# Optimization experiments

Hardware: AMD Instinct MI355X
Metric: run time of the kernel (lower is better)

## Reference

```python
import jax, jax.numpy as jnp
import numpy as np

B, HF, WF = 64, 14, 14
E, D, H, EM, V, L = 2048, 256, 256, 256, 10000, 32


def setup_inputs() -> dict:
    key = jax.random.key(0)
    ks = jax.random.split(key, 16)
    s = lambda k, shape: jax.random.normal(k, shape, jnp.float32) * 0.02
    lengths = jnp.clip(jax.random.randint(ks[2], (B, 1), 2, L + 1), 2, L)
    lengths = lengths.at[0, 0].set(L)  # ensure max target length == L-1 (static)
    return {
        "image_feature": jax.random.normal(ks[0], (B, HF, WF, E), jnp.float32),
        "caption_token": jax.random.randint(ks[1], (B, L), 0, V),
        "caption_length": lengths,
        "Wf": s(ks[3], (E, H)), "bf": jnp.zeros((H,), jnp.float32),
        "Wh": s(ks[4], (D, H)), "bh": jnp.zeros((H,), jnp.float32),
        "We": s(ks[5], (H, 1)), "be": jnp.zeros((1,), jnp.float32),
        "emb": jax.random.uniform(ks[6], (V, EM), jnp.float32, -0.1, 0.1),
        "W_ih": s(ks[7], (EM + E, 4 * D)), "b_ih": jnp.zeros((4 * D,), jnp.float32),
        "W_hh": s(ks[8], (D, 4 * D)), "b_hh": jnp.zeros((4 * D,), jnp.float32),
        "W_hid": s(ks[9], (E, D)), "b_hid": jnp.zeros((D,), jnp.float32),
        "W_cell": s(ks[10], (E, D)), "b_cell": jnp.zeros((D,), jnp.float32),
        "W_gate": s(ks[11], (D, E)), "b_gate": jnp.zeros((E,), jnp.float32),
        "W_head": jax.random.uniform(ks[12], (D, V), jnp.float32, -0.1, 0.1),
        "b_head": jnp.zeros((V,), jnp.float32),
    }


def reference(image_feature, caption_token, caption_length,
              Wf, bf, Wh, bh, We, be, emb,
              W_ih, b_ih, W_hh, b_hh,
              W_hid, b_hid, W_cell, b_cell,
              W_gate, b_gate, W_head, b_head):
    feat = image_feature.reshape(image_feature.shape[0], -1, image_feature.shape[-1])  # [B,P,E]
    lengths = caption_length[:, 0]
    order = jnp.argsort(-lengths)               # descending, stable
    feat = feat[order]
    tok = caption_token[order]
    target = lengths[order] - 1                 # [B] target lengths
    T = tok.shape[1] - 1                        # static max target length

    mean_feat = feat.mean(axis=1)               # [B,E]
    h0 = mean_feat @ W_hid + b_hid              # init hidden
    c0 = mean_feat @ W_cell + b_cell            # init cell
    cap_emb = emb[tok]                          # [B,L,EM] teacher-forcing embeds
    fe = feat @ Wf + bf                         # [B,P,H] feature proj (loop-invariant)

    def step(carry, t):
        h, c = carry
        m = (target > t)[:, None].astype(h.dtype)        # active-row mask (block_size)
        # additive attention
        he = (h @ Wh + bh)[:, None, :]                   # [B,1,H]
        e = jax.nn.relu(fe + he) @ We + be               # [B,P,1]
        w = jax.nn.softmax(e, axis=1)                    # over pixels
        ctx = (w * feat).sum(axis=1)                     # [B,E]
        # sigmoid gate on context
        ctx = jax.nn.sigmoid(h @ W_gate + b_gate) * ctx
        # LSTMCell (torch gate order i,f,g,o)
        x = jnp.concatenate([cap_emb[:, t], ctx], axis=1)
        g = x @ W_ih + b_ih + h @ W_hh + b_hh
        i, f, gg, o = jnp.split(g, 4, axis=1)
        c_new = jax.nn.sigmoid(f) * c + jax.nn.sigmoid(i) * jnp.tanh(gg)
        h_new = jax.nn.sigmoid(o) * jnp.tanh(c_new)
        pred = h_new @ W_head + b_head                   # dropout = identity (eval)
        h = jnp.where(m > 0, h_new, h)
        c = jnp.where(m > 0, c_new, c)
        return (h, c), (pred * m, w[:, :, 0] * m)

    _, (preds, weights) = jax.lax.scan(step, (h0, c0), jnp.arange(T))
    caption_prediction = jnp.transpose(preds, (1, 0, 2))   # [B,T,V]
    attention_weight = jnp.transpose(weights, (1, 0, 2))   # [B,T,P]
    return caption_prediction, attention_weight
```

## Files before the change

kernel.cpp:

```cpp
#include <hip/hip_runtime.h>
#include <math.h>

#define B 64
#define P 196
#define E 2048
#define D 256
#define H_ 256
#define EM 256
#define V 10000
#define L 32
#define T 31
#define KX 2560

__global__ __launch_bounds__(64) void sort_kernel(const int* __restrict__ clen,
                                                  int* __restrict__ order,
                                                  int* __restrict__ target) {
    __shared__ int len_s[B];
    int i = threadIdx.x;
    len_s[i] = clen[i];
    __syncthreads();
    int li = len_s[i];
    int rank = 0;
    for (int j = 0; j < B; ++j) {
        int lj = len_s[j];
        if (lj > li || (lj == li && j < i)) rank++;
    }
    order[rank] = i;
    target[rank] = li - 1;
}

__global__ __launch_bounds__(256) void mean_kernel(const float* __restrict__ feat,
                                                   const int* __restrict__ order,
                                                   float* __restrict__ mean_feat) {
    int b = blockIdx.x;
    int e = blockIdx.y * 256 + threadIdx.x;
    int src = order[b];
    const float* fp = feat + (size_t)src * P * E + e;
    float acc = 0.f;
    #pragma unroll 4
    for (int p = 0; p < P; ++p) acc += fp[(size_t)p * E];
    mean_feat[b * E + e] = acc * (1.0f / (float)P);
}

__global__ __launch_bounds__(256) void h0c0_gemm(const float* __restrict__ mean_feat,
                                                 const float* __restrict__ W_hid,
                                                 const float* __restrict__ W_cell,
                                                 float* __restrict__ hpart) {
    __shared__ float As[32][68];
    __shared__ float Bs[32][64];
    int cb = blockIdx.x;
    int ky = blockIdx.y;
    int tid = threadIdx.x;
    int tx = tid & 15, ty = tid >> 4;
    const float* Wsrc;
    int ncol0;
    if (cb < 4) { Wsrc = W_hid;  ncol0 = cb * 64; }
    else        { Wsrc = W_cell; ncol0 = (cb - 4) * 64; }
    float acc[4][4] = {};
    for (int k0 = ky * 256; k0 < ky * 256 + 256; k0 += 32) {
        #pragma unroll
        for (int q = 0; q < 2; ++q) {
            int idx = q * 256 + tid;
            int kv = idx & 7, m = idx >> 3;
            float4 v = *(const float4*)(mean_feat + (size_t)m * E + k0 + kv * 4);
            As[kv * 4 + 0][m] = v.x;
            As[kv * 4 + 1][m] = v.y;
            As[kv * 4 + 2][m] = v.z;
            As[kv * 4 + 3][m] = v.w;
        }
        #pragma unroll
        for (int q = 0; q < 2; ++q) {
            int idx = q * 256 + tid;
            int n4 = idx & 15, kk = idx >> 4;
            float4 v = *(const float4*)(Wsrc + (size_t)(k0 + kk) * 256 + ncol0 + n4 * 4);
            *(float4*)&Bs[kk][n4 * 4] = v;
        }
        __syncthreads();
        #pragma unroll
        for (int kk = 0; kk < 32; ++kk) {
            float4 av = *(const float4*)&As[kk][ty * 4];
            float4 bv = *(const float4*)&Bs[kk][tx * 4];
            acc[0][0] += av.x * bv.x; acc[0][1] += av.x * bv.y; acc[0][2] += av.x * bv.z; acc[0][3] += av.x * bv.w;
            acc[1][0] += av.y * bv.x; acc[1][1] += av.y * bv.y; acc[1][2] += av.y * bv.z; acc[1][3] += av.y * bv.w;
            acc[2][0] += av.z * bv.x; acc[2][1] += av.z * bv.y; acc[2][2] += av.z * bv.z; acc[2][3] += av.z * bv.w;
            acc[3][0] += av.w * bv.x; acc[3][1] += av.w * bv.y; acc[3][2] += av.w * bv.z; acc[3][3] += av.w * bv.w;
        }
        __syncthreads();
    }
    #pragma unroll
    for (int a = 0; a < 4; ++a) {
        int row = ty * 4 + a;
        float4 o = {acc[a][0], acc[a][1], acc[a][2], acc[a][3]};
        *(float4*)(hpart + ((size_t)ky * B + row) * 512 + cb * 64 + tx * 4) = o;
    }
}

__global__ __launch_bounds__(256) void h0c0_reduce(const float* __restrict__ hpart,
                                                   const float* __restrict__ b_hid,
                                                   const float* __restrict__ b_cell,
                                                   const float* __restrict__ emb,
                                                   const int* __restrict__ cap_tok,
                                                   const int* __restrict__ order,
                                                   float* __restrict__ h,
                                                   float* __restrict__ c,
                                                   float* __restrict__ xbuf) {
    int b = blockIdx.x, tid = threadIdx.x;
    float s0 = 0.f, s1 = 0.f;
    #pragma unroll
    for (int ky = 0; ky < 8; ++ky) {
        const float* hp = hpart + ((size_t)ky * B + b) * 512;
        s0 += hp[tid];
        s1 += hp[256 + tid];
    }
    float h0 = s0 + b_hid[tid];
    h[b * D + tid] = h0;
    c[b * D + tid] = s1 + b_cell[tid];
    xbuf[(size_t)b * KX + 2304 + tid] = h0;
    int tok0 = cap_tok[order[b] * L + 0];
    xbuf[(size_t)b * KX + tid] = emb[(size_t)tok0 * EM + tid];
}

__global__ __launch_bounds__(256) void fe_gemm(const float* __restrict__ feat,
                                               const int* __restrict__ order,
                                               const float* __restrict__ Wf,
                                               const float* __restrict__ bf,
                                               float* __restrict__ fe) {
    __shared__ float As[32][68];
    __shared__ float Bs[32][64];
    __shared__ int srcRow[64];
    int rowBlock = blockIdx.x;
    int colBlock = blockIdx.y;
    int tid = threadIdx.x;
    if (tid < 64) {
        int gr = rowBlock * 64 + tid;
        int b = gr / P, p = gr % P;
        srcRow[tid] = order[b] * P + p;
    }
    __syncthreads();
    int tx = tid & 15, ty = tid >> 4;
    float acc[4][4] = {};
    for (int k0 = 0; k0 < E; k0 += 32) {
        #pragma unroll
        for (int q = 0; q < 2; ++q) {
            int idx = q * 256 + tid;
            int kv = idx & 7, m = idx >> 3;
            float4 v = *(const float4*)(feat + (size_t)srcRow[m] * E + k0 + kv * 4);
            As[kv * 4 + 0][m] = v.x;
            As[kv * 4 + 1][m] = v.y;
            As[kv * 4 + 2][m] = v.z;
            As[kv * 4 + 3][m] = v.w;
        }
        {
            int n4 = tid & 15, kk = tid >> 4;
            float4 v = *(const float4*)(Wf + (size_t)(k0 + kk) * H_ + colBlock * 64 + n4 * 4);
            *(float4*)&Bs[kk][n4 * 4] = v;
            int kk2 = kk + 16;
            float4 v2 = *(const float4*)(Wf + (size_t)(k0 + kk2) * H_ + colBlock * 64 + n4 * 4);
            *(float4*)&Bs[kk2][n4 * 4] = v2;
        }
        __syncthreads();
        #pragma unroll
        for (int kk = 0; kk < 32; ++kk) {
            float4 av = *(const float4*)&As[kk][ty * 4];
            float4 bv = *(const float4*)&Bs[kk][tx * 4];
            acc[0][0] += av.x * bv.x; acc[0][1] += av.x * bv.y; acc[0][2] += av.x * bv.z; acc[0][3] += av.x * bv.w;
            acc[1][0] += av.y * bv.x; acc[1][1] += av.y * bv.y; acc[1][2] += av.y * bv.z; acc[1][3] += av.y * bv.w;
            acc[2][0] += av.z * bv.x; acc[2][1] += av.z * bv.y; acc[2][2] += av.z * bv.z; acc[2][3] += av.z * bv.w;
            acc[3][0] += av.w * bv.x; acc[3][1] += av.w * bv.y; acc[3][2] += av.w * bv.z; acc[3][3] += av.w * bv.w;
        }
        __syncthreads();
    }
    float4 bias = *(const float4*)(bf + colBlock * 64 + tx * 4);
    #pragma unroll
    for (int a = 0; a < 4; ++a) {
        int gr = rowBlock * 64 + ty * 4 + a;
        float4 o;
        o.x = acc[a][0] + bias.x;
        o.y = acc[a][1] + bias.y;
        o.z = acc[a][2] + bias.z;
        o.w = acc[a][3] + bias.w;
        *(float4*)(fe + (size_t)gr * H_ + colBlock * 64 + tx * 4) = o;
    }
}

__global__ __launch_bounds__(256) void attn_pw(const int* __restrict__ target,
                                               const float* __restrict__ gpart,
                                               const float* __restrict__ b_ih,
                                               const float* __restrict__ b_hh,
                                               const float* __restrict__ emb,
                                               const int* __restrict__ cap_tok,
                                               const int* __restrict__ order,
                                               const float* __restrict__ Wh,
                                               const float* __restrict__ bh,
                                               const float* __restrict__ We,
                                               const float* __restrict__ be,
                                               const float* __restrict__ fe,
                                               float* __restrict__ h,
                                               float* __restrict__ c,
                                               float* __restrict__ hn_all,
                                               float* __restrict__ xbuf,
                                               float* __restrict__ wbuf,
                                               float* __restrict__ out2,
                                               int t) {
    int b = blockIdx.x;
    int tgt = target[b];
    bool pw_active = (t > 0) && (tgt > t - 1);
    bool at_active = (tgt > t);
    if (!pw_active && !at_active) return;
    __shared__ float hs[D];
    __shared__ float hes[D];
    __shared__ float es[P];
    __shared__ float red[4];
    int tid = threadIdx.x;
    if (pw_active) {
        int d = tid;
        float gi = b_ih[d] + b_hh[d];
        float gf = b_ih[D + d] + b_hh[D + d];
        float gg = b_ih[2 * D + d] + b_hh[2 * D + d];
        float go = b_ih[3 * D + d] + b_hh[3 * D + d];
        #pragma unroll
        for (int ky = 0; ky < 8; ++ky) {
            const float* gp = gpart + ((size_t)ky * B + b) * 1024;
            gi += gp[d];
            gf += gp[D + d];
            gg += gp[2 * D + d];
            go += gp[3 * D + d];
        }
        float c_old = c[b * D + d];
        float si = 1.f / (1.f + expf(-gi));
        float sf = 1.f / (1.f + expf(-gf));
        float so = 1.f / (1.f + expf(-go));
        float cn = sf * c_old + si * tanhf(gg);
        float hnv = so * tanhf(cn);
        c[b * D + d] = cn;
        h[b * D + d] = hnv;
        hs[d] = hnv;
        hn_all[((size_t)(t - 1) * B + b) * D + d] = hnv;
        xbuf[(size_t)b * KX + 2304 + d] = hnv;
        int tokn = cap_tok[order[b] * L + t];
        xbuf[(size_t)b * KX + d] = emb[(size_t)tokn * EM + d];
    } else {
        hs[tid] = h[b * D + tid];
    }
    __syncthreads();
    if (!at_active) return;
    float acc = 0.f;
    #pragma unroll 8
    for (int k = 0; k < D; ++k) acc += hs[k] * Wh[(size_t)k * H_ + tid];
    hes[tid] = acc + bh[tid];
    __syncthreads();
    int wave = tid >> 6, lane = tid & 63;
    float4 he4 = *(const float4*)&hes[lane * 4];
    float4 we4 = *(const float4*)(We + lane * 4);
    for (int p = wave; p < P; p += 4) {
        float4 fv = *(const float4*)(fe + ((size_t)b * P + p) * H_ + lane * 4);
        float x0 = fv.x + he4.x; x0 = x0 > 0.f ? x0 : 0.f;
        float x1 = fv.y + he4.y; x1 = x1 > 0.f ? x1 : 0.f;
        float x2 = fv.z + he4.z; x2 = x2 > 0.f ? x2 : 0.f;
        float x3 = fv.w + he4.w; x3 = x3 > 0.f ? x3 : 0.f;
        float s = x0 * we4.x + x1 * we4.y + x2 * we4.z + x3 * we4.w;
        #pragma unroll
        for (int off = 32; off > 0; off >>= 1) s += __shfl_down(s, off);
        if (lane == 0) es[p] = s + be[0];
    }
    __syncthreads();
    float mx = -1e30f;
    for (int p = tid; p < P; p += 256) mx = fmaxf(mx, es[p]);
    #pragma unroll
    for (int off = 32; off > 0; off >>= 1) mx = fmaxf(mx, __shfl_down(mx, off));
    if (lane == 0) red[wave] = mx;
    __syncthreads();
    mx = fmaxf(fmaxf(red[0], red[1]), fmaxf(red[2], red[3]));
    __syncthreads();
    float sum = 0.f;
    for (int p = tid; p < P; p += 256) {
        float ex = expf(es[p] - mx);
        es[p] = ex;
        sum += ex;
    }
    #pragma unroll
    for (int off = 32; off > 0; off >>= 1) sum += __shfl_down(sum, off);
    if (lane == 0) red[wave] = sum;
    __syncthreads();
    sum = red[0] + red[1] + red[2] + red[3];
    float inv = 1.0f / sum;
    for (int p = tid; p < P; p += 256) {
        float wv = es[p] * inv;
        wbuf[b * P + p] = wv;
        out2[((size_t)b * T + t) * P + p] = wv;
    }
}

__global__ __launch_bounds__(256) void ctx_kernel(const float* __restrict__ feat,
                                                  const int* __restrict__ order,
                                                  const float* __restrict__ wbuf,
                                                  const float* __restrict__ W_gate,
                                                  const float* __restrict__ b_gate,
                                                  const float* __restrict__ h,
                                                  const int* __restrict__ target,
                                                  float* __restrict__ xbuf,
                                                  int t) {
    int b = blockIdx.x;
    if (target[b] <= t) return;
    int y = blockIdx.y;
    __shared__ float ws_[P];
    __shared__ float hs[D];
    __shared__ float4 rc[3][64];
    __shared__ float4 rg[3][64];
    int tid = threadIdx.x;
    if (tid < P) ws_[tid] = wbuf[b * P + tid];
    hs[tid] = h[b * D + tid];
    __syncthreads();
    int c4 = tid & 63, q = tid >> 6;
    int src = order[b];
    const float4* f4 = (const float4*)(feat + (size_t)src * P * E) + y * 64 + c4;
    float4 acc = {0.f, 0.f, 0.f, 0.f};
    for (int p = q * 49; p < q * 49 + 49; ++p) {
        float w = ws_[p];
        float4 fv = f4[(size_t)p * 512];
        acc.x += w * fv.x; acc.y += w * fv.y; acc.z += w * fv.z; acc.w += w * fv.w;
    }
    const float4* g4 = (const float4*)W_gate + y * 64 + c4;
    float4 gacc = {0.f, 0.f, 0.f, 0.f};
    for (int k = q * 64; k < q * 64 + 64; ++k) {
        float hv = hs[k];
        float4 wv = g4[(size_t)k * 512];
        gacc.x += hv * wv.x; gacc.y += hv * wv.y; gacc.z += hv * wv.z; gacc.w += hv * wv.w;
    }
    if (q) { rc[q - 1][c4] = acc; rg[q - 1][c4] = gacc; }
    __syncthreads();
    if (q == 0) {
        #pragma unroll
        for (int j = 0; j < 3; ++j) {
            float4 a = rc[j][c4], g = rg[j][c4];
            acc.x += a.x; acc.y += a.y; acc.z += a.z; acc.w += a.w;
            gacc.x += g.x; gacc.y += g.y; gacc.z += g.z; gacc.w += g.w;
        }
        float4 gb = *(const float4*)(b_gate + (y * 64 + c4) * 4);
        float4 o;
        o.x = acc.x / (1.f + expf(-(gacc.x + gb.x)));
        o.y = acc.y / (1.f + expf(-(gacc.y + gb.y)));
        o.z = acc.z / (1.f + expf(-(gacc.z + gb.z)));
        o.w = acc.w / (1.f + expf(-(gacc.w + gb.w)));
        *(float4*)(xbuf + (size_t)b * KX + EM + (y * 64 + c4) * 4) = o;
    }
}

__global__ __launch_bounds__(256) void lstm_gemm(const float* __restrict__ xbuf,
                                                 const float* __restrict__ W_ih,
                                                 const float* __restrict__ W_hh,
                                                 float* __restrict__ gpart) {
    __shared__ float As[32][68];
    __shared__ float Bs[32][64];
    int cb = blockIdx.x;
    int ky = blockIdx.y;
    int tid = threadIdx.x;
    int tx = tid & 15, ty = tid >> 4;
    float acc[4][4] = {};
    int k0base = ky * 320;
    for (int k0 = k0base; k0 < k0base + 320; k0 += 32) {
        #pragma unroll
        for (int q = 0; q < 2; ++q) {
            int idx = q * 256 + tid;
            int kv = idx & 7, m = idx >> 3;
            float4 v = *(const float4*)(xbuf + (size_t)m * KX + k0 + kv * 4);
            As[kv * 4 + 0][m] = v.x;
            As[kv * 4 + 1][m] = v.y;
            As[kv * 4 + 2][m] = v.z;
            As[kv * 4 + 3][m] = v.w;
        }
        #pragma unroll
        for (int q = 0; q < 2; ++q) {
            int idx = q * 256 + tid;
            int n4 = idx & 15, kk = idx >> 4;
            int k = k0 + kk;
            const float* src = (k < EM + E) ? (W_ih + (size_t)k * 1024)
                                            : (W_hh + (size_t)(k - EM - E) * 1024);
            float4 v = *(const float4*)(src + cb * 64 + n4 * 4);
            *(float4*)&Bs[kk][n4 * 4] = v;
        }
        __syncthreads();
        #pragma unroll
        for (int kk = 0; kk < 32; ++kk) {
            float4 av = *(const float4*)&As[kk][ty * 4];
            float4 bv = *(const float4*)&Bs[kk][tx * 4];
            acc[0][0] += av.x * bv.x; acc[0][1] += av.x * bv.y; acc[0][2] += av.x * bv.z; acc[0][3] += av.x * bv.w;
            acc[1][0] += av.y * bv.x; acc[1][1] += av.y * bv.y; acc[1][2] += av.y * bv.z; acc[1][3] += av.y * bv.w;
            acc[2][0] += av.z * bv.x; acc[2][1] += av.z * bv.y; acc[2][2] += av.z * bv.z; acc[2][3] += av.z * bv.w;
            acc[3][0] += av.w * bv.x; acc[3][1] += av.w * bv.y; acc[3][2] += av.w * bv.z; acc[3][3] += av.w * bv.w;
        }
        __syncthreads();
    }
    #pragma unroll
    for (int a = 0; a < 4; ++a) {
        int bidx = ty * 4 + a;
        float4 o = {acc[a][0], acc[a][1], acc[a][2], acc[a][3]};
        *(float4*)(gpart + ((size_t)ky * B + bidx) * 1024 + cb * 64 + tx * 4) = o;
    }
}

__global__ __launch_bounds__(256) void head_batch(const float* __restrict__ hn_all,
                                                  const float* __restrict__ W_head,
                                                  const float* __restrict__ b_head,
                                                  const int* __restrict__ target,
                                                  float* __restrict__ out1) {
    int by = blockIdx.y;
    int t = by >> 1, qh = by & 1;
    if (target[qh * 32] <= t) return;
    __shared__ float hs[32][260];
    int cb = blockIdx.x;
    int tid = threadIdx.x;
    #pragma unroll
    for (int q = 0; q < 8; ++q) {
        int idx = q * 256 + tid;
        int r = idx >> 6, kq = idx & 63;
        float4 v = *(const float4*)(hn_all + ((size_t)t * B + qh * 32 + r) * D + kq * 4);
        *(float4*)&hs[r][kq * 4] = v;
    }
    __syncthreads();
    int col = cb * 64 + (tid & 63);
    int rgrp = (tid >> 6) * 8;
    if (col < V) {
        float acc[8] = {};
        for (int kq = 0; kq < 64; ++kq) {
            float w0 = W_head[(size_t)(kq * 4 + 0) * V + col];
            float w1 = W_head[(size_t)(kq * 4 + 1) * V + col];
            float w2 = W_head[(size_t)(kq * 4 + 2) * V + col];
            float w3 = W_head[(size_t)(kq * 4 + 3) * V + col];
            #pragma unroll
            for (int r = 0; r < 8; ++r) {
                float4 hv = *(const float4*)&hs[rgrp + r][kq * 4];
                acc[r] += hv.x * w0 + hv.y * w1 + hv.z * w2 + hv.w * w3;
            }
        }
        float bh_ = b_head[col];
        #pragma unroll
        for (int r = 0; r < 8; ++r) {
            int brow = qh * 32 + rgrp + r;
            if (target[brow] > t)
                out1[((size_t)brow * T + t) * V + col] = acc[r] + bh_;
        }
    }
}

extern "C" void kernel_launch(void* const* d_in, const int* in_sizes, int n_in,
                              void* d_out, int out_size, void* d_ws, size_t ws_size,
                              hipStream_t stream) {
    const float* feat   = (const float*)d_in[0];
    const int*   tok    = (const int*)d_in[1];
    const int*   clen   = (const int*)d_in[2];
    const float* Wf     = (const float*)d_in[3];
    const float* bf     = (const float*)d_in[4];
    const float* Wh     = (const float*)d_in[5];
    const float* bh     = (const float*)d_in[6];
    const float* We     = (const float*)d_in[7];
    const float* be     = (const float*)d_in[8];
    const float* emb    = (const float*)d_in[9];
    const float* W_ih   = (const float*)d_in[10];
    const float* b_ih   = (const float*)d_in[11];
    const float* W_hh   = (const float*)d_in[12];
    const float* b_hh   = (const float*)d_in[13];
    const float* W_hid  = (const float*)d_in[14];
    const float* b_hid  = (const float*)d_in[15];
    const float* W_cell = (const float*)d_in[16];
    const float* b_cell = (const float*)d_in[17];
    const float* W_gate = (const float*)d_in[18];
    const float* b_gate = (const float*)d_in[19];
    const float* W_head = (const float*)d_in[20];
    const float* b_head = (const float*)d_in[21];

    float* out1 = (float*)d_out;
    float* out2 = out1 + (size_t)B * T * V;

    char* wp = (char*)d_ws;
    int* order   = (int*)wp;           wp += 256;
    int* targetp = (int*)wp;           wp += 256;
    float* fe    = (float*)wp;         wp += (size_t)B * P * H_ * sizeof(float);
    float* hbuf  = (float*)wp;         wp += (size_t)B * D * sizeof(float);
    float* cbuf  = (float*)wp;         wp += (size_t)B * D * sizeof(float);
    float* wbuf  = (float*)wp;         wp += (size_t)B * P * sizeof(float);
    float* xbuf  = (float*)wp;         wp += (size_t)B * KX * sizeof(float);
    float* gpart = (float*)wp;         wp += (size_t)8 * B * 1024 * sizeof(float);
    float* mean_feat = (float*)wp;     wp += (size_t)B * E * sizeof(float);
    float* hpart = (float*)wp;         wp += (size_t)8 * B * 512 * sizeof(float);
    float* hn_all = (float*)wp;        wp += (size_t)T * B * D * sizeof(float);

    hipMemsetAsync(d_out, 0, (size_t)out_size * sizeof(float), stream);

    sort_kernel<<<1, 64, 0, stream>>>(clen, order, targetp);
    mean_kernel<<<dim3(B, E / 256), 256, 0, stream>>>(feat, order, mean_feat);
    h0c0_gemm<<<dim3(8, 8), 256, 0, stream>>>(mean_feat, W_hid, W_cell, hpart);
    h0c0_reduce<<<B, 256, 0, stream>>>(hpart, b_hid, b_cell, emb, tok, order,
                                       hbuf, cbuf, xbuf);
    fe_gemm<<<dim3(196, 4), 256, 0, stream>>>(feat, order, Wf, bf, fe);

    for (int t = 0; t < T; ++t) {
        attn_pw<<<B, 256, 0, stream>>>(targetp, gpart, b_ih, b_hh, emb, tok, order,
                                       Wh, bh, We, be, fe, hbuf, cbuf, hn_all,
                                       xbuf, wbuf, out2, t);
        ctx_kernel<<<dim3(B, 8), 256, 0, stream>>>(feat, order, wbuf, W_gate, b_gate,
                                                   hbuf, targetp, xbuf, t);
        lstm_gemm<<<dim3(16, 8), 256, 0, stream>>>(xbuf, W_ih, W_hh, gpart);
    }
    attn_pw<<<B, 256, 0, stream>>>(targetp, gpart, b_ih, b_hh, emb, tok, order,
                                   Wh, bh, We, be, fe, hbuf, cbuf, hn_all,
                                   xbuf, wbuf, out2, T);
    head_batch<<<dim3(157, 62), 256, 0, stream>>>(hn_all, W_head, b_head, targetp, out1);
}
```

Measured before the change: 2.873 ms.

## Fuse all stages into one persistent cooperative kernel with grid syncs

Replaces the many per-timestep kernel launches with a single cooperative persistent kernel that loops over phases, separated by grid-wide syncs. The fe GEMM and mean reduction run in the same phase, and the output head projection for step t-1 is overlapped with the LSTM GEMM of step t rather than done as one batched GEMM at the end. The fe tile is widened to 64x128. This removes launch overhead across the 31-step recurrence. In exchange it depends on grid.sync cost and on a grid size capped at 512 blocks, which limits parallelism in the large GEMM phases.

```diff
diff --git a/kernel.cpp b/kernel.cpp
--- a/kernel.cpp
+++ b/kernel.cpp
@@ -1,5 +1,8 @@
 #include <hip/hip_runtime.h>
+#include <hip/hip_cooperative_groups.h>
 #include <math.h>
+
+namespace cg = cooperative_groups;
 
 #define B 64
 #define P 196
@@ -12,78 +15,112 @@
 #define T 31
 #define KX 2560
 
-__global__ __launch_bounds__(64) void sort_kernel(const int* __restrict__ clen,
-                                                  int* __restrict__ order,
-                                                  int* __restrict__ target) {
-    __shared__ int len_s[B];
-    int i = threadIdx.x;
-    len_s[i] = clen[i];
-    __syncthreads();
-    int li = len_s[i];
-    int rank = 0;
-    for (int j = 0; j < B; ++j) {
-        int lj = len_s[j];
-        if (lj > li || (lj == li && j < i)) rank++;
-    }
-    order[rank] = i;
-    target[rank] = li - 1;
-}
-
-__global__ __launch_bounds__(256) void mean_kernel(const float* __restrict__ feat,
-                                                   const int* __restrict__ order,
-                                                   float* __restrict__ mean_feat) {
-    int b = blockIdx.x;
-    int e = blockIdx.y * 256 + threadIdx.x;
-    int src = order[b];
-    const float* fp = feat + (size_t)src * P * E + e;
-    float acc = 0.f;
-    #pragma unroll 4
-    for (int p = 0; p < P; ++p) acc += fp[(size_t)p * E];
-    mean_feat[b * E + e] = acc * (1.0f / (float)P);
-}
-
-__global__ __launch_bounds__(256) void h0c0_gemm(const float* __restrict__ mean_feat,
-                                                 const float* __restrict__ W_hid,
-                                                 const float* __restrict__ W_cell,
-                                                 float* __restrict__ hpart) {
-    __shared__ float As[32][68];
-    __shared__ float Bs[32][64];
-    int cb = blockIdx.x;
-    int ky = blockIdx.y;
-    int tid = threadIdx.x;
+struct Params {
+    const float* feat; const int* tok; const int* clen;
+    const float* Wf; const float* bf; const float* Wh; const float* bh;
+    const float* We; const float* be; const float* emb;
+    const float* W_ih; const float* b_ih; const float* W_hh; const float* b_hh;
+    const float* W_hid; const float* b_hid; const float* W_cell; const float* b_cell;
+    const float* W_gate; const float* b_gate; const float* W_head; const float* b_head;
+    float* out1; float* out2;
+    int* order; int* target;
+    float* fe; float* h; float* c; float* wbuf; float* xbuf;
+    float* gpart; float* mean_feat; float* hpart; float* hn_all;
+};
+
+__device__ __forceinline__ void fe_tile(const Params& p, int task, int tid, float* sm) {
+    float* As = sm;
+    float* Bs = sm + 2176;
+    int* srcRow = (int*)(sm + 6272);
+    int rb = task >> 1, cb = task & 1;
+    __syncthreads();
+    if (tid < 64) {
+        int gr = rb * 64 + tid;
+        int b = gr / P, pp = gr % P;
+        srcRow[tid] = p.order[b] * P + pp;
+    }
+    __syncthreads();
     int tx = tid & 15, ty = tid >> 4;
-    const float* Wsrc;
-    int ncol0;
-    if (cb < 4) { Wsrc = W_hid;  ncol0 = cb * 64; }
-    else        { Wsrc = W_cell; ncol0 = (cb - 4) * 64; }
+    float acc[4][8] = {};
+    for (int k0 = 0; k0 < E; k0 += 32) {
+        #pragma unroll
+        for (int q = 0; q < 2; ++q) {
+            int idx = q * 256 + tid;
+            int kv = idx & 7, m = idx >> 3;
+            float4 v = *(const float4*)(p.feat + (size_t)srcRow[m] * E + k0 + kv * 4);
+            As[(kv*4+0)*68+m] = v.x; As[(kv*4+1)*68+m] = v.y;
+            As[(kv*4+2)*68+m] = v.z; As[(kv*4+3)*68+m] = v.w;
+        }
+        #pragma unroll
+        for (int q = 0; q < 4; ++q) {
+            int idx = q * 256 + tid;
+            int n4 = idx & 31, kk = idx >> 5;
+            float4 v = *(const float4*)(p.Wf + (size_t)(k0+kk)*H_ + cb*128 + n4*4);
+            *(float4*)&Bs[kk*128 + n4*4] = v;
+        }
+        __syncthreads();
+        #pragma unroll
+        for (int kk = 0; kk < 32; ++kk) {
+            float4 av = *(const float4*)&As[kk*68 + ty*4];
+            float4 b0 = *(const float4*)&Bs[kk*128 + tx*8];
+            float4 b1 = *(const float4*)&Bs[kk*128 + tx*8 + 4];
+            float a_[4] = {av.x, av.y, av.z, av.w};
+            float b_[8] = {b0.x,b0.y,b0.z,b0.w,b1.x,b1.y,b1.z,b1.w};
+            #pragma unroll
+            for (int r = 0; r < 4; ++r)
+                #pragma unroll
+                for (int cc = 0; cc < 8; ++cc)
+                    acc[r][cc] += a_[r] * b_[cc];
+        }
+        __syncthreads();
+    }
+    float4 bias0 = *(const float4*)(p.bf + cb*128 + tx*8);
+    float4 bias1 = *(const float4*)(p.bf + cb*128 + tx*8 + 4);
+    #pragma unroll
+    for (int r = 0; r < 4; ++r) {
+        int gr = rb * 64 + ty * 4 + r;
+        float4 o0 = {acc[r][0]+bias0.x, acc[r][1]+bias0.y, acc[r][2]+bias0.z, acc[r][3]+bias0.w};
+        float4 o1 = {acc[r][4]+bias1.x, acc[r][5]+bias1.y, acc[r][6]+bias1.z, acc[r][7]+bias1.w};
+        *(float4*)(p.fe + (size_t)gr * H_ + cb*128 + tx*8) = o0;
+        *(float4*)(p.fe + (size_t)gr * H_ + cb*128 + tx*8 + 4) = o1;
+    }
+}
+
+__device__ __forceinline__ void h0c0_tile(const Params& p, int task, int tid, float* sm) {
+    float* As = sm;
+    float* Bs = sm + 2176;
+    int cb = task >> 3, ky = task & 7;
+    const float* Wsrc; int ncol0;
+    if (cb < 4) { Wsrc = p.W_hid;  ncol0 = cb * 64; }
+    else        { Wsrc = p.W_cell; ncol0 = (cb - 4) * 64; }
+    int tx = tid & 15, ty = tid >> 4;
     float acc[4][4] = {};
+    __syncthreads();
     for (int k0 = ky * 256; k0 < ky * 256 + 256; k0 += 32) {
         #pragma unroll
         for (int q = 0; q < 2; ++q) {
             int idx = q * 256 + tid;
             int kv = idx & 7, m = idx >> 3;
-            float4 v = *(const float4*)(mean_feat + (size_t)m * E + k0 + kv * 4);
-            As[kv * 4 + 0][m] = v.x;
-            As[kv * 4 + 1][m] = v.y;
-            As[kv * 4 + 2][m] = v.z;
-            As[kv * 4 + 3][m] = v.w;
+            float4 v = *(const float4*)(p.mean_feat + (size_t)m * E + k0 + kv * 4);
+            As[(kv*4+0)*68+m] = v.x; As[(kv*4+1)*68+m] = v.y;
+            As[(kv*4+2)*68+m] = v.z; As[(kv*4+3)*68+m] = v.w;
         }
         #pragma unroll
         for (int q = 0; q < 2; ++q) {
             int idx = q * 256 + tid;
             int n4 = idx & 15, kk = idx >> 4;
             float4 v = *(const float4*)(Wsrc + (size_t)(k0 + kk) * 256 + ncol0 + n4 * 4);
-            *(float4*)&Bs[kk][n4 * 4] = v;
+            *(float4*)&Bs[kk*64 + n4*4] = v;
         }
         __syncthreads();
         #pragma unroll
         for (int kk = 0; kk < 32; ++kk) {
-            float4 av = *(const float4*)&As[kk][ty * 4];
-            float4 bv = *(const float4*)&Bs[kk][tx * 4];
-            acc[0][0] += av.x * bv.x; acc[0][1] += av.x * bv.y; acc[0][2] += av.x * bv.z; acc[0][3] += av.x * bv.w;
-            acc[1][0] += av.y * bv.x; acc[1][1] += av.y * bv.y; acc[1][2] += av.y * bv.z; acc[1][3] += av.y * bv.w;
-            acc[2][0] += av.z * bv.x; acc[2][1] += av.z * bv.y; acc[2][2] += av.z * bv.z; acc[2][3] += av.z * bv.w;
-            acc[3][0] += av.w * bv.x; acc[3][1] += av.w * bv.y; acc[3][2] += av.w * bv.z; acc[3][3] += av.w * bv.w;
+            float4 av = *(const float4*)&As[kk*68 + ty*4];
+            float4 bv = *(const float4*)&Bs[kk*64 + tx*4];
+            acc[0][0] += av.x*bv.x; acc[0][1] += av.x*bv.y; acc[0][2] += av.x*bv.z; acc[0][3] += av.x*bv.w;
+            acc[1][0] += av.y*bv.x; acc[1][1] += av.y*bv.y; acc[1][2] += av.y*bv.z; acc[1][3] += av.y*bv.w;
+            acc[2][0] += av.z*bv.x; acc[2][1] += av.z*bv.y; acc[2][2] += av.z*bv.z; acc[2][3] += av.z*bv.w;
+            acc[3][0] += av.w*bv.x; acc[3][1] += av.w*bv.y; acc[3][2] += av.w*bv.z; acc[3][3] += av.w*bv.w;
         }
         __syncthreads();
     }
@@ -91,169 +128,74 @@
     for (int a = 0; a < 4; ++a) {
         int row = ty * 4 + a;
         float4 o = {acc[a][0], acc[a][1], acc[a][2], acc[a][3]};
-        *(float4*)(hpart + ((size_t)ky * B + row) * 512 + cb * 64 + tx * 4) = o;
-    }
-}
-
-__global__ __launch_bounds__(256) void h0c0_reduce(const float* __restrict__ hpart,
-                                                   const float* __restrict__ b_hid,
-                                                   const float* __restrict__ b_cell,
-                                                   const float* __restrict__ emb,
-                                                   const int* __restrict__ cap_tok,
-                                                   const int* __restrict__ order,
-                                                   float* __restrict__ h,
-                                                   float* __restrict__ c,
-                                                   float* __restrict__ xbuf) {
-    int b = blockIdx.x, tid = threadIdx.x;
+        *(float4*)(p.hpart + ((size_t)ky * B + row) * 512 + cb * 64 + tx * 4) = o;
+    }
+}
+
+__device__ __forceinline__ void reduce_task(const Params& p, int b, int tid) {
     float s0 = 0.f, s1 = 0.f;
     #pragma unroll
     for (int ky = 0; ky < 8; ++ky) {
-        const float* hp = hpart + ((size_t)ky * B + b) * 512;
-        s0 += hp[tid];
-        s1 += hp[256 + tid];
-    }
-    float h0 = s0 + b_hid[tid];
-    h[b * D + tid] = h0;
-    c[b * D + tid] = s1 + b_cell[tid];
-    xbuf[(size_t)b * KX + 2304 + tid] = h0;
-    int tok0 = cap_tok[order[b] * L + 0];
-    xbuf[(size_t)b * KX + tid] = emb[(size_t)tok0 * EM + tid];
-}
-
-__global__ __launch_bounds__(256) void fe_gemm(const float* __restrict__ feat,
-                                               const int* __restrict__ order,
-                                               const float* __restrict__ Wf,
-                                               const float* __restrict__ bf,
-                                               float* __restrict__ fe) {
-    __shared__ float As[32][68];
-    __shared__ float Bs[32][64];
-    __shared__ int srcRow[64];
-    int rowBlock = blockIdx.x;
-    int colBlock = blockIdx.y;
-    int tid = threadIdx.x;
-    if (tid < 64) {
-        int gr = rowBlock * 64 + tid;
-        int b = gr / P, p = gr % P;
-        srcRow[tid] = order[b] * P + p;
-    }
-    __syncthreads();
-    int tx = tid & 15, ty = tid >> 4;
-    float acc[4][4] = {};
-    for (int k0 = 0; k0 < E; k0 += 32) {
-        #pragma unroll
-        for (int q = 0; q < 2; ++q) {
-            int idx = q * 256 + tid;
-            int kv = idx & 7, m = idx >> 3;
-            float4 v = *(const float4*)(feat + (size_t)srcRow[m] * E + k0 + kv * 4);
-            As[kv * 4 + 0][m] = v.x;
-            As[kv * 4 + 1][m] = v.y;
-            As[kv * 4 + 2][m] = v.z;
-            As[kv * 4 + 3][m] = v.w;
-        }
-        {
-            int n4 = tid & 15, kk = tid >> 4;
-            float4 v = *(const float4*)(Wf + (size_t)(k0 + kk) * H_ + colBlock * 64 + n4 * 4);
-            *(float4*)&Bs[kk][n4 * 4] = v;
-            int kk2 = kk + 16;
-            float4 v2 = *(const float4*)(Wf + (size_t)(k0 + kk2) * H_ + colBlock * 64 + n4 * 4);
-            *(float4*)&Bs[kk2][n4 * 4] = v2;
-        }
-        __syncthreads();
-        #pragma unroll
-        for (int kk = 0; kk < 32; ++kk) {
-            float4 av = *(const float4*)&As[kk][ty * 4];
-            float4 bv = *(const float4*)&Bs[kk][tx * 4];
-            acc[0][0] += av.x * bv.x; acc[0][1] += av.x * bv.y; acc[0][2] += av.x * bv.z; acc[0][3] += av.x * bv.w;
-            acc[1][0] += av.y * bv.x; acc[1][1] += av.y * bv.y; acc[1][2] += av.y * bv.z; acc[1][3] += av.y * bv.w;
-            acc[2][0] += av.z * bv.x; acc[2][1] += av.z * bv.y; acc[2][2] += av.z * bv.z; acc[2][3] += av.z * bv.w;
-            acc[3][0] += av.w * bv.x; acc[3][1] += av.w * bv.y; acc[3][2] += av.w * bv.z; acc[3][3] += av.w * bv.w;
-        }
-        __syncthreads();
-    }
-    float4 bias = *(const float4*)(bf + colBlock * 64 + tx * 4);
-    #pragma unroll
-    for (int a = 0; a < 4; ++a) {
-        int gr = rowBlock * 64 + ty * 4 + a;
-        float4 o;
-        o.x = acc[a][0] + bias.x;
-        o.y = acc[a][1] + bias.y;
-        o.z = acc[a][2] + bias.z;
-        o.w = acc[a][3] + bias.w;
-        *(float4*)(fe + (size_t)gr * H_ + colBlock * 64 + tx * 4) = o;
-    }
-}
-
-__global__ __launch_bounds__(256) void attn_pw(const int* __restrict__ target,
-                                               const float* __restrict__ gpart,
-                                               const float* __restrict__ b_ih,
-                                               const float* __restrict__ b_hh,
-                                               const float* __restrict__ emb,
-                                               const int* __restrict__ cap_tok,
-                                               const int* __restrict__ order,
-                                               const float* __restrict__ Wh,
-                                               const float* __restrict__ bh,
-                                               const float* __restrict__ We,
-                                               const float* __restrict__ be,
-                                               const float* __restrict__ fe,
-                                               float* __restrict__ h,
-                                               float* __restrict__ c,
-                                               float* __restrict__ hn_all,
-                                               float* __restrict__ xbuf,
-                                               float* __restrict__ wbuf,
-                                               float* __restrict__ out2,
-                                               int t) {
-    int b = blockIdx.x;
-    int tgt = target[b];
+        const float* hp = p.hpart + ((size_t)ky * B + b) * 512;
+        s0 += hp[tid]; s1 += hp[256 + tid];
+    }
+    float h0 = s0 + p.b_hid[tid];
+    p.h[b * D + tid] = h0;
+    p.c[b * D + tid] = s1 + p.b_cell[tid];
+    p.xbuf[(size_t)b * KX + 2304 + tid] = h0;
+    int tok0 = p.tok[p.order[b] * L + 0];
+    p.xbuf[(size_t)b * KX + tid] = p.emb[(size_t)tok0 * EM + tid];
+}
+
+__device__ __forceinline__ void attn_pw_phase(const Params& p, int t, int b, int tid, float* sm) {
+    float* hs  = sm;
+    float* hes = sm + 256;
+    float* es  = sm + 512;
+    float* red = sm + 712;
+    int tgt = p.target[b];
     bool pw_active = (t > 0) && (tgt > t - 1);
     bool at_active = (tgt > t);
     if (!pw_active && !at_active) return;
-    __shared__ float hs[D];
-    __shared__ float hes[D];
-    __shared__ float es[P];
-    __shared__ float red[4];
-    int tid = threadIdx.x;
+    __syncthreads();
     if (pw_active) {
         int d = tid;
-        float gi = b_ih[d] + b_hh[d];
-        float gf = b_ih[D + d] + b_hh[D + d];
-        float gg = b_ih[2 * D + d] + b_hh[2 * D + d];
-        float go = b_ih[3 * D + d] + b_hh[3 * D + d];
+        float gi = p.b_ih[d] + p.b_hh[d];
+        float gf = p.b_ih[D + d] + p.b_hh[D + d];
+        float gg = p.b_ih[2 * D + d] + p.b_hh[2 * D + d];
+        float go = p.b_ih[3 * D + d] + p.b_hh[3 * D + d];
         #pragma unroll
         for (int ky = 0; ky < 8; ++ky) {
-            const float* gp = gpart + ((size_t)ky * B + b) * 1024;
-            gi += gp[d];
-            gf += gp[D + d];
-            gg += gp[2 * D + d];
-            go += gp[3 * D + d];
-        }
-        float c_old = c[b * D + d];
+            const float* gp = p.gpart + ((size_t)ky * B + b) * 1024;
+            gi += gp[d]; gf += gp[D + d]; gg += gp[2 * D + d]; go += gp[3 * D + d];
+        }
+        float c_old = p.c[b * D + d];
         float si = 1.f / (1.f + expf(-gi));
         float sf = 1.f / (1.f + expf(-gf));
         float so = 1.f / (1.f + expf(-go));
         float cn = sf * c_old + si * tanhf(gg);
         float hnv = so * tanhf(cn);
-        c[b * D + d] = cn;
-        h[b * D + d] = hnv;
+        p.c[b * D + d] = cn;
+        p.h[b * D + d] = hnv;
         hs[d] = hnv;
-        hn_all[((size_t)(t - 1) * B + b) * D + d] = hnv;
-        xbuf[(size_t)b * KX + 2304 + d] = hnv;
-        int tokn = cap_tok[order[b] * L + t];
-        xbuf[(size_t)b * KX + d] = emb[(size_t)tokn * EM + d];
+        p.hn_all[((size_t)(t - 1) * B + b) * D + d] = hnv;
+        p.xbuf[(size_t)b * KX + 2304 + d] = hnv;
+        int tokn = p.tok[p.order[b] * L + t];
+        p.xbuf[(size_t)b * KX + d] = p.emb[(size_t)tokn * EM + d];
     } else {
-        hs[tid] = h[b * D + tid];
+        hs[tid] = p.h[b * D + tid];
     }
     __syncthreads();
     if (!at_active) return;
     float acc = 0.f;
     #pragma unroll 8
-    for (int k = 0; k < D; ++k) acc += hs[k] * Wh[(size_t)k * H_ + tid];
-    hes[tid] = acc + bh[tid];
+    for (int k = 0; k < D; ++k) acc += hs[k] * p.Wh[(size_t)k * H_ + tid];
+    hes[tid] = acc + p.bh[tid];
     __syncthreads();
     int wave = tid >> 6, lane = tid & 63;
     float4 he4 = *(const float4*)&hes[lane * 4];
-    float4 we4 = *(const float4*)(We + lane * 4);
-    for (int p = wave; p < P; p += 4) {
-        float4 fv = *(const float4*)(fe + ((size_t)b * P + p) * H_ + lane * 4);
+    float4 we4 = *(const float4*)(p.We + lane * 4);
+    for (int pp = wave; pp < P; pp += 4) {
+        float4 fv = *(const float4*)(p.fe + ((size_t)b * P + pp) * H_ + lane * 4);
         float x0 = fv.x + he4.x; x0 = x0 > 0.f ? x0 : 0.f;
         float x1 = fv.y + he4.y; x1 = x1 > 0.f ? x1 : 0.f;
         float x2 = fv.z + he4.z; x2 = x2 > 0.f ? x2 : 0.f;
@@ -261,11 +203,11 @@
         float s = x0 * we4.x + x1 * we4.y + x2 * we4.z + x3 * we4.w;
         #pragma unroll
         for (int off = 32; off > 0; off >>= 1) s += __shfl_down(s, off);
-        if (lane == 0) es[p] = s + be[0];
+        if (lane == 0) es[pp] = s + p.be[0];
     }
     __syncthreads();
     float mx = -1e30f;
-    for (int p = tid; p < P; p += 256) mx = fmaxf(mx, es[p]);
+    for (int pp = tid; pp < P; pp += 256) mx = fmaxf(mx, es[pp]);
     #pragma unroll
     for (int off = 32; off > 0; off >>= 1) mx = fmaxf(mx, __shfl_down(mx, off));
     if (lane == 0) red[wave] = mx;
@@ -273,9 +215,9 @@
     mx = fmaxf(fmaxf(red[0], red[1]), fmaxf(red[2], red[3]));
     __syncthreads();
     float sum = 0.f;
-    for (int p = tid; p < P; p += 256) {
-        float ex = expf(es[p] - mx);
-        es[p] = ex;
+    for (int pp = tid; pp < P; pp += 256) {
+        float ex = expf(es[pp] - mx);
+        es[pp] = ex;
         sum += ex;
     }
     #pragma unroll
@@ -284,110 +226,93 @@
     __syncthreads();
     sum = red[0] + red[1] + red[2] + red[3];
     float inv = 1.0f / sum;
-    for (int p = tid; p < P; p += 256) {
-        float wv = es[p] * inv;
-        wbuf[b * P + p] = wv;
-        out2[((size_t)b * T + t) * P + p] = wv;
-    }
-}
-
-__global__ __launch_bounds__(256) void ctx_kernel(const float* __restrict__ feat,
-                                                  const int* __restrict__ order,
-                                                  const float* __restrict__ wbuf,
-                                                  const float* __restrict__ W_gate,
-                                                  const float* __restrict__ b_gate,
-                                                  const float* __restrict__ h,
-                                                  const int* __restrict__ target,
-                                                  float* __restrict__ xbuf,
-                                                  int t) {
-    int b = blockIdx.x;
-    if (target[b] <= t) return;
-    int y = blockIdx.y;
-    __shared__ float ws_[P];
-    __shared__ float hs[D];
-    __shared__ float4 rc[3][64];
-    __shared__ float4 rg[3][64];
-    int tid = threadIdx.x;
-    if (tid < P) ws_[tid] = wbuf[b * P + tid];
-    hs[tid] = h[b * D + tid];
+    for (int pp = tid; pp < P; pp += 256) {
+        float wv = es[pp] * inv;
+        p.wbuf[b * P + pp] = wv;
+        p.out2[((size_t)b * T + t) * P + pp] = wv;
+    }
+}
+
+__device__ __forceinline__ void ctx_phase(const Params& p, int t, int b, int y, int tid, float* sm) {
+    if (p.target[b] <= t) return;
+    float* ws_ = sm;
+    float* hs  = sm + 196;
+    float4* rc = (float4*)(sm + 464);
+    float4* rg = (float4*)(sm + 464 + 768);
+    __syncthreads();
+    if (tid < P) ws_[tid] = p.wbuf[b * P + tid];
+    hs[tid] = p.h[b * D + tid];
     __syncthreads();
     int c4 = tid & 63, q = tid >> 6;
-    int src = order[b];
-    const float4* f4 = (const float4*)(feat + (size_t)src * P * E) + y * 64 + c4;
+    int src = p.order[b];
+    const float4* f4 = (const float4*)(p.feat + (size_t)src * P * E) + y * 64 + c4;
     float4 acc = {0.f, 0.f, 0.f, 0.f};
-    for (int p = q * 49; p < q * 49 + 49; ++p) {
-        float w = ws_[p];
-        float4 fv = f4[(size_t)p * 512];
+    for (int pp = q * 49; pp < q * 49 + 49; ++pp) {
+        float w = ws_[pp];
+        float4 fv = f4[(size_t)pp * 512];
         acc.x += w * fv.x; acc.y += w * fv.y; acc.z += w * fv.z; acc.w += w * fv.w;
     }
-    const float4* g4 = (const float4*)W_gate + y * 64 + c4;
+    const float4* g4 = (const float4*)p.W_gate + y * 64 + c4;
     float4 gacc = {0.f, 0.f, 0.f, 0.f};
     for (int k = q * 64; k < q * 64 + 64; ++k) {
         float hv = hs[k];
         float4 wv = g4[(size_t)k * 512];
         gacc.x += hv * wv.x; gacc.y += hv * wv.y; gacc.z += hv * wv.z; gacc.w += hv * wv.w;
     }
-    if (q) { rc[q - 1][c4] = acc; rg[q - 1][c4] = gacc; }
+    if (q) { rc[(q - 1) * 64 + c4] = acc; rg[(q - 1) * 64 + c4] = gacc; }
     __syncthreads();
     if (q == 0) {
         #pragma unroll
         for (int j = 0; j < 3; ++j) {
-            float4 a = rc[j][c4], g = rg[j][c4];
+            float4 a = rc[j * 64 + c4], g = rg[j * 64 + c4];
             acc.x += a.x; acc.y += a.y; acc.z += a.z; acc.w += a.w;
             gacc.x += g.x; gacc.y += g.y; gacc.z += g.z; gacc.w += g.w;
         }
-        float4 gb = *(const float4*)(b_gate + (y * 64 + c4) * 4);
+        float4 gb = *(const float4*)(p.b_gate + (y * 64 + c4) * 4);
         float4 o;
         o.x = acc.x / (1.f + expf(-(gacc.x + gb.x)));
         o.y = acc.y / (1.f + expf(-(gacc.y + gb.y)));
         o.z = acc.z / (1.f + expf(-(gacc.z + gb.z)));
         o.w = acc.w / (1.f + expf(-(gacc.w + gb.w)));
-        *(float4*)(xbuf + (size_t)b * KX + EM + (y * 64 + c4) * 4) = o;
-    }
-}
-
-__global__ __launch_bounds__(256) void lstm_gemm(const float* __restrict__ xbuf,
-                                                 const float* __restrict__ W_ih,
-                                                 const float* __restrict__ W_hh,
-                                                 float* __restrict__ gpart) {
-    __shared__ float As[32][68];
-    __shared__ float Bs[32][64];
-    int cb = blockIdx.x;
-    int ky = blockIdx.y;
-    int tid = threadIdx.x;
+        *(float4*)(p.xbuf + (size_t)b * KX + EM + (y * 64 + c4) * 4) = o;
+    }
+}
+
+__device__ __forceinline__ void lstm_tile(const Params& p, int cb, int ky, int tid, float* sm) {
+    float* As = sm;
+    float* Bs = sm + 2176;
     int tx = tid & 15, ty = tid >> 4;
     float acc[4][4] = {};
     int k0base = ky * 320;
+    __syncthreads();
     for (int k0 = k0base; k0 < k0base + 320; k0 += 32) {
         #pragma unroll
         for (int q = 0; q < 2; ++q) {
             int idx = q * 256 + tid;
             int kv = idx & 7, m = idx >> 3;
-            float4 v = *(const float4*)(xbuf + (size_t)m * KX + k0 + kv * 4);
-            As[kv * 4 + 0][m] = v.x;
-            As[kv * 4 + 1][m] = v.y;
-            As[kv * 4 + 2][m] = v.z;
-            As[kv * 4 + 3][m] = v.w;
+            float4 v = *(const float4*)(p.xbuf + (size_t)m * KX + k0 + kv * 4);
+            As[(kv*4+0)*68+m] = v.x; As[(kv*4+1)*68+m] = v.y;
+            As[(kv*4+2)*68+m] = v.z; As[(kv*4+3)*68+m] = v.w;
         }
         #pragma unroll
         for (int q = 0; q < 2; ++q) {
             int idx = q * 256 + tid;
             int n4 = idx & 15, kk = idx >> 4;
             int k = k0 + kk;
-            const float* src = (k < EM + E) ? (W_ih + (size_t)k * 1024)
-                                            : (W_hh + (size_t)(k - EM - E) * 1024);
+            const float* src = (k < EM + E) ? (p.W_ih + (size_t)k * 1024)
+                                            : (p.W_hh + (size_t)(k - EM - E) * 1024);
             float4 v = *(const float4*)(src + cb * 64 + n4 * 4);
-            *(float4*)&Bs[kk][n4 * 4] = v;
+            *(float4*)&Bs[kk*64 + n4*4] = v;
         }
         __syncthreads();
         #pragma unroll
         for (int kk = 0; kk < 32; ++kk) {
-            float4 av = *(const float4*)&As[kk][ty * 4];
-            float4 bv = *(const float4*)&Bs[kk][tx * 4];
-            acc[0][0] += av.x * bv.x; acc[0][1] += av.x * bv.y; acc[0][2] += av.x * bv.z; acc[0][3] += av.x * bv.w;
-            acc[1][0] += av.y * bv.x; acc[1][1] += av.y * bv.y; acc[1][2] += av.y * bv.z; acc[1][3] += av.y * bv.w;
-            acc[2][0] += av.z * bv.x; acc[2][1] += av.z * bv.y; acc[2][2] += av.z * bv.z; acc[2][3] += av.z * bv.w;
-            acc[3][0] += av.w * bv.x; acc[3][1] += av.w * bv.y; acc[3][2] += av.w * bv.z; acc[3][3] += av.w * bv.w;
+            float4 av = *(const float4*)&As[kk*68 + ty*4];
+            float4 bv = *(const float4*)&Bs[kk*64 + tx*4];
+            acc[0][0] += av.x*bv.x; acc[0][1] += av.x*bv.y; acc[0][2] += av.x*bv.z; acc[0][3] += av.x*bv.w;
+            acc[1][0] += av.y*bv.x; acc[1][1] += av.y*bv.y; acc[1][2] += av.y*bv.z; acc[1][3] += av.y*bv.w;
+            acc[2][0] += av.z*bv.x; acc[2][1] += av.z*bv.y; acc[2][2] += av.z*bv.z; acc[2][3] += av.z*bv.w;
+            acc[3][0] += av.w*bv.x; acc[3][1] += av.w*bv.y; acc[3][2] += av.w*bv.z; acc[3][3] += av.w*bv.w;
         }
         __syncthreads();
     }
@@ -395,27 +320,21 @@
     for (int a = 0; a < 4; ++a) {
         int bidx = ty * 4 + a;
         float4 o = {acc[a][0], acc[a][1], acc[a][2], acc[a][3]};
-        *(float4*)(gpart + ((size_t)ky * B + bidx) * 1024 + cb * 64 + tx * 4) = o;
-    }
-}
-
-__global__ __launch_bounds__(256) void head_batch(const float* __restrict__ hn_all,
-                                                  const float* __restrict__ W_head,
-                                                  const float* __restrict__ b_head,
-                                                  const int* __restrict__ target,
-                                                  float* __restrict__ out1) {
-    int by = blockIdx.y;
-    int t = by >> 1, qh = by & 1;
-    if (target[qh * 32] <= t) return;
-    __shared__ float hs[32][260];
-    int cb = blockIdx.x;
-    int tid = threadIdx.x;
+        *(float4*)(p.gpart + ((size_t)ky * B + bidx) * 1024 + cb * 64 + tx * 4) = o;
+    }
+}
+
+__device__ __forceinline__ void head_tile(const Params& p, int t, int id, int tid, float* sm) {
+    int cb = id % 157, qh = id / 157;
+    if (p.target[qh * 32] <= t) return;
+    float* hs = sm;
+    __syncthreads();
     #pragma unroll
     for (int q = 0; q < 8; ++q) {
         int idx = q * 256 + tid;
         int r = idx >> 6, kq = idx & 63;
-        float4 v = *(const float4*)(hn_all + ((size_t)t * B + qh * 32 + r) * D + kq * 4);
-        *(float4*)&hs[r][kq * 4] = v;
+        float4 v = *(const float4*)(p.hn_all + ((size_t)t * B + qh * 32 + r) * D + kq * 4);
+        *(float4*)&hs[r * 256 + kq * 4] = v;
     }
     __syncthreads();
     int col = cb * 64 + (tid & 63);
@@ -423,87 +342,142 @@
     if (col < V) {
         float acc[8] = {};
         for (int kq = 0; kq < 64; ++kq) {
-            float w0 = W_head[(size_t)(kq * 4 + 0) * V + col];
-            float w1 = W_head[(size_t)(kq * 4 + 1) * V + col];
-            float w2 = W_head[(size_t)(kq * 4 + 2) * V + col];
-            float w3 = W_head[(size_t)(kq * 4 + 3) * V + col];
+            float w0 = p.W_head[(size_t)(kq * 4 + 0) * V + col];
+            float w1 = p.W_head[(size_t)(kq * 4 + 1) * V + col];
+            float w2 = p.W_head[(size_t)(kq * 4 + 2) * V + col];
+            float w3 = p.W_head[(size_t)(kq * 4 + 3) * V + col];
             #pragma unroll
             for (int r = 0; r < 8; ++r) {
-                float4 hv = *(const float4*)&hs[rgrp + r][kq * 4];
+                float4 hv = *(const float4*)&hs[(rgrp + r) * 256 + kq * 4];
                 acc[r] += hv.x * w0 + hv.y * w1 + hv.z * w2 + hv.w * w3;
             }
         }
-        float bh_ = b_head[col];
+        float bh_ = p.b_head[col];
         #pragma unroll
         for (int r = 0; r < 8; ++r) {
             int brow = qh * 32 + rgrp + r;
-            if (target[brow] > t)
-                out1[((size_t)brow * T + t) * V + col] = acc[r] + bh_;
-        }
-    }
+            if (p.target[brow] > t)
+                p.out1[((size_t)brow * T + t) * V + col] = acc[r] + bh_;
+        }
+    }
+}
+
+__global__ __launch_bounds__(256, 2) void mega(Params p) {
+    cg::grid_group grid = cg::this_grid();
+    __shared__ __align__(16) float sm[8192];
+    int blk = blockIdx.x, tid = threadIdx.x;
+    int G = gridDim.x;
+
+    if (blk == 0) {
+        int* lens = (int*)sm;
+        if (tid < B) lens[tid] = p.clen[tid];
+        __syncthreads();
+        if (tid < B) {
+            int li = lens[tid], rank = 0;
+            for (int j = 0; j < B; ++j) {
+                int lj = lens[j];
+                if (lj > li || (lj == li && j < tid)) rank++;
+            }
+            p.order[rank] = tid;
+            p.target[rank] = li - 1;
+        }
+    }
+    grid.sync();
+
+    for (int task = blk; task < 904; task += G) {
+        if (task < 392) {
+            fe_tile(p, task, tid, sm);
+        } else {
+            int mt = task - 392;
+            int b = mt >> 3, e0 = (mt & 7) << 8;
+            int src = p.order[b];
+            const float* fp = p.feat + (size_t)src * P * E + e0 + tid;
+            float acc = 0.f;
+            #pragma unroll 4
+            for (int pp = 0; pp < P; ++pp) acc += fp[(size_t)pp * E];
+            p.mean_feat[b * E + e0 + tid] = acc * (1.0f / 196.0f);
+        }
+    }
+    grid.sync();
+
+    for (int task = blk; task < 64; task += G) h0c0_tile(p, task, tid, sm);
+    grid.sync();
+
+    for (int task = blk; task < 64; task += G) reduce_task(p, task, tid);
+    grid.sync();
+
+    for (int t = 0; t < T; ++t) {
+        for (int task = blk; task < B; task += G) attn_pw_phase(p, t, task, tid, sm);
+        grid.sync();
+        for (int task = blk; task < 512; task += G) ctx_phase(p, t, task >> 3, task & 7, tid, sm);
+        grid.sync();
+        for (int task = blk; task < 442; task += G) {
+            if (task < 128) lstm_tile(p, task & 15, task >> 4, tid, sm);
+            else if (t >= 1) head_tile(p, t - 1, task - 128, tid, sm);
+        }
+        grid.sync();
+    }
+    for (int task = blk; task < B; task += G) attn_pw_phase(p, T, task, tid, sm);
+    grid.sync();
+    for (int task = blk; task < 314; task += G) head_tile(p, T - 1, task, tid, sm);
 }
 
 extern "C" void kernel_launch(void* const* d_in, const int* in_sizes, int n_in,
                               void* d_out, int out_size, void* d_ws, size_t ws_size,
                               hipStream_t stream) {
-    const float* feat   = (const float*)d_in[0];
-    const int*   tok    = (const int*)d_in[1];
-    const int*   clen   = (const int*)d_in[2];
-    const float* Wf     = (const float*)d_in[3];
-    const float* bf     = (const float*)d_in[4];
-    const float* Wh     = (const float*)d_in[5];
-    const float* bh     = (const float*)d_in[6];
-    const float* We     = (const float*)d_in[7];
-    const float* be     = (const float*)d_in[8];
-    const float* emb    = (const float*)d_in[9];
-    const float* W_ih   = (const float*)d_in[10];
-    const float* b_ih   = (const float*)d_in[11];
-    const float* W_hh   = (const float*)d_in[12];
-    const float* b_hh   = (const float*)d_in[13];
-    const float* W_hid  = (const float*)d_in[14];
-    const float* b_hid  = (const float*)d_in[15];
-    const float* W_cell = (const float*)d_in[16];
-    const float* b_cell = (const float*)d_in[17];
-    const float* W_gate = (const float*)d_in[18];
-    const float* b_gate = (const float*)d_in[19];
-    const float* W_head = (const float*)d_in[20];
-    const float* b_head = (const float*)d_in[21];
-
-    float* out1 = (float*)d_out;
-    float* out2 = out1 + (size_t)B * T * V;
+    Params p;
+    p.feat   = (const float*)d_in[0];
+    p.tok    = (const int*)d_in[1];
+    p.clen   = (const int*)d_in[2];
+    p.Wf     = (const float*)d_in[3];
+    p.bf     = (const float*)d_in[4];
+    p.Wh     = (const float*)d_in[5];
+    p.bh     = (const float*)d_in[6];
+    p.We     = (const float*)d_in[7];
+    p.be     = (const float*)d_in[8];
+    p.emb    = (const float*)d_in[9];
+    p.W_ih   = (const float*)d_in[10];
+    p.b_ih   = (const float*)d_in[11];
+    p.W_hh   = (const float*)d_in[12];
+    p.b_hh   = (const float*)d_in[13];
+    p.W_hid  = (const float*)d_in[14];
+    p.b_hid  = (const float*)d_in[15];
+    p.W_cell = (const float*)d_in[16];
+    p.b_cell = (const float*)d_in[17];
+    p.W_gate = (const float*)d_in[18];
+    p.b_gate = (const float*)d_in[19];
+    p.W_head = (const float*)d_in[20];
+    p.b_head = (const float*)d_in[21];
+
+    p.out1 = (float*)d_out;
+    p.out2 = p.out1 + (size_t)B * T * V;
 
     char* wp = (char*)d_ws;
-    int* order   = (int*)wp;           wp += 256;
-    int* targetp = (int*)wp;           wp += 256;
-    float* fe    = (float*)wp;         wp += (size_t)B * P * H_ * sizeof(float);
-    float* hbuf  = (float*)wp;         wp += (size_t)B * D * sizeof(float);
-    float* cbuf  = (float*)wp;         wp += (size_t)B * D * sizeof(float);
-    float* wbuf  = (float*)wp;         wp += (size_t)B * P * sizeof(float);
-    float* xbuf  = (float*)wp;         wp += (size_t)B * KX * sizeof(float);
-    float* gpart = (float*)wp;         wp += (size_t)8 * B * 1024 * sizeof(float);
-    float* mean_feat = (float*)wp;     wp += (size_t)B * E * sizeof(float);
-    float* hpart = (float*)wp;         wp += (size_t)8 * B * 512 * sizeof(float);
-    float* hn_all = (float*)wp;        wp += (size_t)T * B * D * sizeof(float);
+    p.order   = (int*)wp;            wp += 256;
+    p.target  = (int*)wp;            wp += 256;
+    p.fe      = (float*)wp;          wp += (size_t)B * P * H_ * sizeof(float);
+    p.h       = (float*)wp;          wp += (size_t)B * D * sizeof(float);
+    p.c       = (float*)wp;          wp += (size_t)B * D * sizeof(float);
+    p.wbuf    = (float*)wp;          wp += (size_t)B * P * sizeof(float);
+    p.xbuf    = (float*)wp;          wp += (size_t)B * KX * sizeof(float);
+    p.gpart   = (float*)wp;          wp += (size_t)8 * B * 1024 * sizeof(float);
+    p.mean_feat = (float*)wp;        wp += (size_t)B * E * sizeof(float);
+    p.hpart   = (float*)wp;          wp += (size_t)8 * B * 512 * sizeof(float);
+    p.hn_all  = (float*)wp;          wp += (size_t)T * B * D * sizeof(float);
 
     hipMemsetAsync(d_out, 0, (size_t)out_size * sizeof(float), stream);
 
-    sort_kernel<<<1, 64, 0, stream>>>(clen, order, targetp);
-    mean_kernel<<<dim3(B, E / 256), 256, 0, stream>>>(feat, order, mean_feat);
-    h0c0_gemm<<<dim3(8, 8), 256, 0, stream>>>(mean_feat, W_hid, W_cell, hpart);
-    h0c0_reduce<<<B, 256, 0, stream>>>(hpart, b_hid, b_cell, emb, tok, order,
-                                       hbuf, cbuf, xbuf);
-    fe_gemm<<<dim3(196, 4), 256, 0, stream>>>(feat, order, Wf, bf, fe);
-
-    for (int t = 0; t < T; ++t) {
-        attn_pw<<<B, 256, 0, stream>>>(targetp, gpart, b_ih, b_hh, emb, tok, order,
-                                       Wh, bh, We, be, fe, hbuf, cbuf, hn_all,
-                                       xbuf, wbuf, out2, t);
-        ctx_kernel<<<dim3(B, 8), 256, 0, stream>>>(feat, order, wbuf, W_gate, b_gate,
-                                                   hbuf, targetp, xbuf, t);
-        lstm_gemm<<<dim3(16, 8), 256, 0, stream>>>(xbuf, W_ih, W_hh, gpart);
-    }
-    attn_pw<<<B, 256, 0, stream>>>(targetp, gpart, b_ih, b_hh, emb, tok, order,
-                                   Wh, bh, We, be, fe, hbuf, cbuf, hn_all,
-                                   xbuf, wbuf, out2, T);
-    head_batch<<<dim3(157, 62), 256, 0, stream>>>(hn_all, W_head, b_head, targetp, out1);
-}
+    int dev = 0;
+    hipGetDevice(&dev);
+    int numCU = 256;
+    hipDeviceGetAttribute(&numCU, hipDeviceAttributeMultiprocessorCount, dev);
+    int maxBlocksPerCU = 0;
+    hipOccupancyMaxActiveBlocksPerMultiprocessor(&maxBlocksPerCU, (const void*)mega, 256, 0);
+    if (maxBlocksPerCU < 1) maxBlocksPerCU = 1;
+    long long g = (long long)maxBlocksPerCU * (long long)numCU;
+    if (g > 512) g = 512;
+    if (g < 64) g = 64;
+
+    void* kargs[] = { (void*)&p };
+    hipLaunchCooperativeKernel((const void*)mega, dim3((unsigned)g), dim3(256), kargs, 0, stream);
+}
```

Result: slower. 10.20 ms (+255.1%).
